# Kernel tuning notes

Measured on AMD Instinct MI355X. Metric: run time of the kernel, lower is better.

## Reference

```python
import jax, jax.numpy as jnp
import numpy as np

N_NODES = 8192
NNZ = 131072

def spmm(idx, vals, M):
    # sparse (n,n) @ dense (n,m) -> (n,m) via edge-list gather + segment-sum
    rows, cols = idx[0], idx[1]
    return jax.ops.segment_sum(vals[:, None] * M[cols], rows, num_segments=N_NODES)

def gw_conv(A_list, X, Z, W):
    # X: (B, d, n) node features; Z: (n, dz); W: (d, out)
    B, d, n = X.shape
    X0 = X.reshape(-1, n)          # (B*d, n)
    Xt = X0.T                      # (n, B*d)
    total_t = Xt                   # sum over Chebyshev-order slices (batched path sums concat dim)
    for idx, vals in A_list:
        X1t = spmm(idx, vals, Xt)                 # order-1 diffusion
        X2t = 2.0 * spmm(idx, vals, X1t) - Xt     # Chebyshev order-2 recursion
        total_t = total_t + X1t + X2t
    # adaptive dense attention adjacency, softmax over dim 0 (columns)
    Az = jax.nn.softmax(jax.nn.relu(Z @ Z.T), axis=0)  # (n, n)
    total_t = total_t + Az @ Xt
    Xr = total_t.T.reshape(B, d, n).transpose(0, 2, 1)  # (B, n, d)
    return Xr @ W                                       # (B, n, out)

def setup_inputs() -> dict:
    key = jax.random.key(0)
    ks = jax.random.split(key, 8)
    d_in, h0, h1 = 64, 128, 128
    inp = {
        "A1_indices": jax.random.randint(ks[0], (2, NNZ), 0, N_NODES, dtype=jnp.int64) if jax.config.jax_enable_x64 else jax.random.randint(ks[0], (2, NNZ), 0, N_NODES, dtype=jnp.int32),
        "A1_values": jax.random.uniform(ks[1], (NNZ,), dtype=jnp.float32),
        "A2_indices": jax.random.randint(ks[2], (2, NNZ), 0, N_NODES, dtype=jnp.int32),
        "A2_values": jax.random.uniform(ks[3], (NNZ,), dtype=jnp.float32),
        "X": jax.random.normal(ks[4], (8, d_in, N_NODES), dtype=jnp.float32),
        "Z": jax.random.normal(ks[5], (N_NODES, 64), dtype=jnp.float32),
        "W1": jax.random.normal(ks[6], (d_in, h0), dtype=jnp.float32) / np.sqrt(h0),
        "W2": jax.random.normal(ks[7], (h0, h1), dtype=jnp.float32) / np.sqrt(h1),
    }
    return inp

def reference(A1_indices, A1_values, A2_indices, A2_values, X, Z, W1, W2):
    A = [(A1_indices, A1_values), (A2_indices, A2_values)]
    H = jax.nn.relu(gw_conv(A, X, Z, W1).transpose(0, 2, 1))  # (B, h0, n)
    H = jax.nn.relu(gw_conv(A, H, Z, W2).transpose(0, 2, 1))  # (B, h1, n)
    return H.mean(axis=2)                                     # aggregate over nodes -> (B, h1)
```

## Files before the change

kernel.cpp:

```cpp
#include <hip/hip_runtime.h>


#define NN 8192
#define NNZE 131072
#define CSHIFT 48.0f

typedef float4 f4;
typedef __attribute__((ext_vector_type(8))) short bf16x8;
typedef __attribute__((ext_vector_type(4))) float f32x4;

typedef __attribute__((address_space(3))) short lds_short;
typedef __attribute__((address_space(1))) const short glb_short;

struct P8s { short* p[8]; };

__device__ inline short f2b(float x){
  unsigned u = __float_as_uint(x);
  unsigned r = (u + 0x7fffu + ((u >> 16) & 1u)) >> 16;
  return (short)r;
}
__device__ inline float b2f(unsigned short b){
  return __uint_as_float(((unsigned)b) << 16);
}

__global__ __launch_bounds__(256) void k_count2(const int* __restrict__ i1, const int* __restrict__ i2,
                                                int* __restrict__ c1, int* __restrict__ c2){
  int e = blockIdx.x*256 + threadIdx.x;
  if (blockIdx.y == 0) atomicAdd(&c1[i1[e]], 1);
  else                 atomicAdd(&c2[i2[e]], 1);
}

__global__ __launch_bounds__(1024) void k_scan2(const int* __restrict__ cnt1, const int* __restrict__ cnt2,
                                                int* __restrict__ ptr1, int* __restrict__ ptr2,
                                                int* __restrict__ cur1, int* __restrict__ cur2){
  __shared__ int sums[1024];
  const int* cnt = blockIdx.x ? cnt2 : cnt1;
  int* ptr = blockIdx.x ? ptr2 : ptr1;
  int* cur = blockIdx.x ? cur2 : cur1;
  int t = threadIdx.x;
  int loc[8]; int s = 0;
  #pragma unroll
  for (int i=0;i<8;i++){ loc[i]=s; s += cnt[t*8+i]; }
  sums[t]=s; __syncthreads();
  for (int off=1; off<1024; off<<=1){
    int v = (t>=off) ? sums[t-off] : 0;
    __syncthreads();
    sums[t] += v;
    __syncthreads();
  }
  int excl = sums[t]-s;
  #pragma unroll
  for (int i=0;i<8;i++){ int v = excl + loc[i]; ptr[t*8+i] = v; cur[t*8+i] = v; }
  if (t==1023) ptr[NN] = sums[1023];
}

__global__ __launch_bounds__(256) void k_fill2(const int* __restrict__ i1, const float* __restrict__ v1,
                                               const int* __restrict__ i2, const float* __restrict__ v2,
                                               int* __restrict__ cur1, int* __restrict__ cur2,
                                               int* __restrict__ cidx1, float* __restrict__ cval1,
                                               int* __restrict__ cidx2, float* __restrict__ cval2){
  int e = blockIdx.x*256 + threadIdx.x;
  const int* idx; const float* vals; int* cur; int* cidx; float* cval;
  if (blockIdx.y == 0){ idx=i1; vals=v1; cur=cur1; cidx=cidx1; cval=cval1; }
  else                { idx=i2; vals=v2; cur=cur2; cidx=cidx2; cval=cval2; }
  int r = idx[e], c = idx[NNZE+e];
  int p = atomicAdd(&cur[r], 1);
  cidx[p] = c; cval[p] = vals[e];
}

template<int R>
__global__ __launch_bounds__(256) void k_transb(const float* __restrict__ src, short* __restrict__ dstb){
  __shared__ float tile[32][33];
  int tx = threadIdx.x & 31, ty = threadIdx.x >> 5;
  int j0 = blockIdx.x*32, f0 = blockIdx.y*32;
  #pragma unroll
  for (int u=0;u<32;u+=8) tile[ty+u][tx] = src[(size_t)(f0+ty+u)*NN + j0+tx];
  __syncthreads();
  #pragma unroll
  for (int u=0;u<32;u+=8) dstb[(size_t)(j0+ty+u)*R + f0+tx] = f2b(tile[tx][ty+u]);
}

__global__ __launch_bounds__(256) void k_zb(const float* __restrict__ Z, short* __restrict__ Zb){
  int i = blockIdx.x*256 + threadIdx.x;
  Zb[i] = f2b(Z[i]);
}

__global__ __launch_bounds__(256) void k_wt(const float* __restrict__ W1, const float* __restrict__ W2,
                                            short* __restrict__ W1t, short* __restrict__ W2t){
  int t = threadIdx.x;
  if (blockIdx.x == 0){
    for (int i=t; i<64*128; i+=256){ int k=i>>7, o=i&127; W1t[o*64+k] = f2b(W1[i]); }
  } else {
    for (int i=t; i<128*128; i+=256){ int k=i>>7, o=i&127; W2t[o*128+k] = f2b(W2[i]); }
  }
}

__global__ __launch_bounds__(512) void k_colsum_mfma(const short* __restrict__ Zb, float* __restrict__ sb){
  int t = threadIdx.x;
  int w = t >> 6, l = t & 63;
  int lo = l & 15, g = l >> 4;
  int j = blockIdx.x*128 + w*16 + lo;
  const bf16x8* Zb8 = (const bf16x8*)Zb;
  bf16x8 bj0 = Zb8[j*8 + g];
  bf16x8 bj1 = Zb8[j*8 + g + 4];
  int i0 = blockIdx.y * (NN/8);
  float sum = 0.f;
  for (int i = i0; i < i0 + NN/8; i += 16){
    bf16x8 a0 = Zb8[(size_t)(i+lo)*8 + g];
    bf16x8 a1 = Zb8[(size_t)(i+lo)*8 + g + 4];
    f32x4 s = (f32x4){0.f,0.f,0.f,0.f};
    s = __builtin_amdgcn_mfma_f32_16x16x32_bf16(a0, bj0, s, 0,0,0);
    s = __builtin_amdgcn_mfma_f32_16x16x32_bf16(a1, bj1, s, 0,0,0);
    #pragma unroll
    for (int r=0;r<4;r++) sum += __expf(s[r] - CSHIFT);
  }
  sum += __shfl_xor(sum, 16);
  sum += __shfl_xor(sum, 32);
  if (g == 0) atomicAdd(sb + j, sum);
}

__global__ __launch_bounds__(256) void k_scaleb(const float* __restrict__ X, const float* __restrict__ sb,
                                                short* __restrict__ Yt){
  int i = blockIdx.x*256 + threadIdx.x;
  int node4 = i & (NN/4 - 1);
  f4 x = ((const f4*)X)[i];
  f4 sv = ((const f4*)sb)[node4];
  short4 o;
  o.x = f2b(x.x*(1.0f/sv.x)); o.y = f2b(x.y*(1.0f/sv.y));
  o.z = f2b(x.z*(1.0f/sv.z)); o.w = f2b(x.w*(1.0f/sv.w));
  ((short4*)Yt)[i] = o;
}

template<int F, int MODE>
__global__ __launch_bounds__(512, 4) void k_fused(
    const short* __restrict__ Zb, const short* __restrict__ YS, P8s pp, int ksize, int kzbase, int nattn,
    const int* __restrict__ ptr1, const int* __restrict__ cidx1, const float* __restrict__ cval1,
    const int* __restrict__ ptr2, const int* __restrict__ cidx2, const float* __restrict__ cval2,
    const short* __restrict__ g1, const short* __restrict__ g2, const short* __restrict__ gy,
    short* __restrict__ so1, short* __restrict__ so2, float* __restrict__ T)
{
  __shared__ __align__(16) short zk[2][32*64];
  __shared__ __align__(16) short yt[2][256*32];
  __shared__ __align__(16) short p_lds[128*40];
  int t = threadIdx.x;

  if ((int)blockIdx.x < nattn){
    constexpr int NBY = F/256;
    int id0 = blockIdx.x;
    int id = (id0 & 7)*32 + (id0 >> 3);
    int bx = id & 63, rest = id >> 6;
    int m0 = bx * 128;
    int n0 = (rest % NBY) * 256;
    int kz = kzbase + rest / NBY;
    int kbeg = kz * ksize, kend = kbeg + ksize;
    int w = t >> 6, l = t & 63;
    int lo = l & 15, g = l >> 4;
    int wm = w >> 2, wn = w & 3;

    const bf16x8* Zb8 = (const bf16x8*)Zb;
    int zirow = m0 + w*16 + lo;
    bf16x8 ziA0 = Zb8[(size_t)zirow*8 + g];
    bf16x8 ziA1 = Zb8[(size_t)zirow*8 + g + 4];

    f32x4 acc[4][4];
    #pragma unroll
    for (int i=0;i<4;i++)
      #pragma unroll
      for (int j=0;j<4;j++) acc[i][j] = (f32x4){0.f,0.f,0.f,0.f};

    auto STAGE = [&](int b, int kk){
      if (t < 256){
        int r = t >> 3, c = t & 7;
        const short* src = Zb + (((size_t)(kk + r)) << 6) + ((c ^ (r & 7)) << 3);
        __builtin_amdgcn_global_load_lds((glb_short*)src, (lds_short*)&zk[b][t*8], 16, 0, 0);
      }
      #pragma unroll
      for (int p=0;p<2;p++){
        int cc = p*512 + t;
        int r = cc >> 2, c = cc & 3;
        const short* src = YS + (size_t)(n0 + r)*NN + kk + ((c ^ ((r >> 1) & 3)) << 3);
        __builtin_amdgcn_global_load_lds((glb_short*)src, (lds_short*)&yt[b][cc*8], 16, 0, 0);
      }
    };

    STAGE(0, kbeg);

    int cur = 0;
    for (int k0 = kbeg; k0 < kend; k0 += 32){
      asm volatile("s_waitcnt vmcnt(0)" ::: "memory");
      __builtin_amdgcn_s_barrier();
      __builtin_amdgcn_sched_barrier(0);
      if (k0 + 32 < kend) STAGE(cur ^ 1, k0 + 32);
      int xa = g ^ (lo & 7), xb = (g + 4) ^ (lo & 7);
      bf16x8 b00 = *(const bf16x8*)&zk[cur][(lo*8 + xa)*8];
      bf16x8 b01 = *(const bf16x8*)&zk[cur][(lo*8 + xb)*8];
      bf16x8 b10 = *(const bf16x8*)&zk[cur][((16+lo)*8 + xa)*8];
      bf16x8 b11 = *(const bf16x8*)&zk[cur][((16+lo)*8 + xb)*8];
      f32x4 s0 = (f32x4){0.f,0.f,0.f,0.f};
      f32x4 s1 = (f32x4){0.f,0.f,0.f,0.f};
      s0 = __builtin_amdgcn_mfma_f32_16x16x32_bf16(ziA0, b00, s0, 0,0,0);
      s0 = __builtin_amdgcn_mfma_f32_16x16x32_bf16(ziA1, b01, s0, 0,0,0);
      s1 = __builtin_amdgcn_mfma_f32_16x16x32_bf16(ziA0, b10, s1, 0,0,0);
      s1 = __builtin_amdgcn_mfma_f32_16x16x32_bf16(ziA1, b11, s1, 0,0,0);
      int prow = w*16 + g*4;
      #pragma unroll
      for (int r=0;r<4;r++){
        p_lds[(prow+r)*40 + lo]      = f2b(__expf(s0[r] - CSHIFT));
        p_lds[(prow+r)*40 + 16 + lo] = f2b(__expf(s1[r] - CSHIFT));
      }
      asm volatile("s_waitcnt lgkmcnt(0)" ::: "memory");
      __builtin_amdgcn_s_barrier();
      bf16x8 aP[4];
      #pragma unroll
      for (int mf=0; mf<4; mf++)
        aP[mf] = *(const bf16x8*)&p_lds[(wm*64 + mf*16 + lo)*40 + g*8];
      __builtin_amdgcn_s_setprio(1);
      #pragma unroll
      for (int nf=0; nf<4; nf++){
        int nl = wn*64 + nf*16 + lo;
        bf16x8 bY = *(const bf16x8*)&yt[cur][(nl*4 + (g ^ ((nl >> 1) & 3)))*8];
        #pragma unroll
        for (int mf=0; mf<4; mf++)
          acc[mf][nf] = __builtin_amdgcn_mfma_f32_16x16x32_bf16(aP[mf], bY, acc[mf][nf], 0,0,0);
      }
      __builtin_amdgcn_s_setprio(0);
      cur ^= 1;
    }
    short* outp = pp.p[kz];
    #pragma unroll
    for (int mf=0; mf<4; mf++){
      int row = m0 + wm*64 + mf*16 + g*4;
      #pragma unroll
      for (int nf=0; nf<4; nf++){
        int col = n0 + wn*64 + nf*16 + lo;
        #pragma unroll
        for (int r=0;r<4;r++)
          outp[(size_t)(row+r)*F + col] = f2b(acc[mf][nf][r]);
      }
    }
  } else {
    constexpr int LPR = F/8;
    constexpr int RPB = 512/LPR;
    int gid = blockIdx.x - nattn;
    int ts = t % LPR, rl = t / LPR;
    if (MODE == 0){
      constexpr int M = NN/RPB;
      int mat = gid / M;
      int blk = gid - mat*M;
      const int*   ptr  = mat ? ptr2  : ptr1;
      const int*   cidx = mat ? cidx2 : cidx1;
      const float* cval = mat ? cval2 : cval1;
      short* outb = mat ? so2 : so1;
      int r = blk*RPB + rl;
      const bf16x8* Y8 = (const bf16x8*)g1;
      int p0 = ptr[r], p1 = ptr[r+1];
      float a[8];
      #pragma unroll
      for (int j=0;j<8;j++) a[j]=0.f;
      int p = p0;
      for (; p+7 < p1; p += 8){
        int   c[8]; float v[8]; bf16x8 x[8];
        #pragma unroll
        for (int q=0;q<8;q++){ c[q]=cidx[p+q]; v[q]=cval[p+q]; }
        #pragma unroll
        for (int q=0;q<8;q++) x[q] = Y8[(size_t)c[q]*LPR + ts];
        #pragma unroll
        for (int q=0;q<8;q++)
          #pragma unroll
          for (int j=0;j<8;j++) a[j] += v[q]*b2f((unsigned short)x[q][j]);
      }
      for (; p < p1; ++p){
        int c0 = cidx[p]; float v0 = cval[p];
        bf16x8 x0 = Y8[(size_t)c0*LPR + ts];
        #pragma unroll
        for (int j=0;j<8;j++) a[j] += v0*b2f((unsigned short)x0[j]);
      }
      bf16x8 o;
      #pragma unroll
      for (int j=0;j<8;j++) o[j] = f2b(a[j]);
      ((bf16x8*)outb)[(size_t)r*LPR + ts] = o;
    } else {
      int r = gid*RPB + rl;
      const bf16x8* Xa = (const bf16x8*)g1;
      const bf16x8* Xb = (const bf16x8*)g2;
      float a[8];
      #pragma unroll
      for (int j=0;j<8;j++) a[j]=0.f;
      {
        int p0 = ptr1[r], p1 = ptr1[r+1];
        int p = p0;
        for (; p+7 < p1; p += 8){
          int   c[8]; float v[8]; bf16x8 x[8];
          #pragma unroll
          for (int q=0;q<8;q++){ c[q]=cidx1[p+q]; v[q]=cval1[p+q]; }
          #pragma unroll
          for (int q=0;q<8;q++) x[q] = Xa[(size_t)c[q]*LPR + ts];
          #pragma unroll
          for (int q=0;q<8;q++)
            #pragma unroll
            for (int j=0;j<8;j++) a[j] += v[q]*b2f((unsigned short)x[q][j]);
        }
        for (; p < p1; ++p){
          int c0 = cidx1[p]; float v0 = cval1[p];
          bf16x8 x0 = Xa[(size_t)c0*LPR + ts];
          #pragma unroll
          for (int j=0;j<8;j++) a[j] += v0*b2f((unsigned short)x0[j]);
        }
      }
      {
        int p0 = ptr2[r], p1 = ptr2[r+1];
        int p = p0;
        for (; p+7 < p1; p += 8){
          int   c[8]; float v[8]; bf16x8 x[8];
          #pragma unroll
          for (int q=0;q<8;q++){ c[q]=cidx2[p+q]; v[q]=cval2[p+q]; }
          #pragma unroll
          for (int q=0;q<8;q++) x[q] = Xb[(size_t)c[q]*LPR + ts];
          #pragma unroll
          for (int q=0;q<8;q++)
            #pragma unroll
            for (int j=0;j<8;j++) a[j] += v[q]*b2f((unsigned short)x[q][j]);
        }
        for (; p < p1; ++p){
          int c0 = cidx2[p]; float v0 = cval2[p];
          bf16x8 x0 = Xb[(size_t)c0*LPR + ts];
          #pragma unroll
          for (int j=0;j<8;j++) a[j] += v0*b2f((unsigned short)x0[j]);
        }
      }
      bf16x8 sa = Xa[(size_t)r*LPR + ts];
      bf16x8 sbv = Xb[(size_t)r*LPR + ts];
      bf16x8 yv = ((const bf16x8*)gy)[(size_t)r*LPR + ts];
      float o[8];
      #pragma unroll
      for (int j=0;j<8;j++)
        o[j] = 2.f*a[j] + b2f((unsigned short)sa[j]) + b2f((unsigned short)sbv[j]) - b2f((unsigned short)yv[j]);
      size_t o4 = ((size_t)r*F + ts*8) >> 2;
      ((f4*)T)[o4]   = (f4){o[0],o[1],o[2],o[3]};
      ((f4*)T)[o4+1] = (f4){o[4],o[5],o[6],o[7]};
    }
  }
}

__global__ __launch_bounds__(512) void k_headm_mfma(
    const float* __restrict__ T, P8s parts, const short* __restrict__ W1t,
    const float* __restrict__ sbv, short* __restrict__ Hb, short* __restrict__ Yt)
{
  __shared__ __align__(16) short hl[128*136];
  __shared__ float rsl[128];
  int t = threadIdx.x;
  int j0 = blockIdx.x*128, b = blockIdx.y;
  for (int u = t; u < 1024; u += 512){
    int row = u >> 3, c = u & 7;
    size_t base = (size_t)(j0+row)*512 + b*64 + c*8;
    f4 x0 = *(const f4*)(T + base);
    f4 x1 = *(const f4*)(T + base + 4);
    float v[8] = {x0.x,x0.y,x0.z,x0.w,x1.x,x1.y,x1.z,x1.w};
    #pragma unroll
    for (int j=0;j<4;j++){
      bf16x8 p = *(const bf16x8*)(parts.p[j] + base);
      #pragma unroll
      for (int q=0;q<8;q++) v[q] += b2f((unsigned short)p[q]);
    }
    bf16x8 o;
    #pragma unroll
    for (int q=0;q<8;q++) o[q] = f2b(v[q]);
    *(bf16x8*)&hl[(row*8 + (c ^ (row & 7)))*8] = o;
  }
  if (t < 128) rsl[t] = 1.0f / sbv[j0 + t];
  __syncthreads();
  int w = t >> 6, l = t & 63, lo = l & 15, g = l >> 4;
  int arow = w*16 + lo;
  f32x4 acc[8];
  #pragma unroll
  for (int nf=0;nf<8;nf++) acc[nf] = (f32x4){0.f,0.f,0.f,0.f};
  #pragma unroll
  for (int ks=0; ks<2; ks++){
    bf16x8 aA = *(const bf16x8*)&hl[(arow*8 + ((ks*4+g) ^ (arow & 7)))*8];
    #pragma unroll
    for (int nf=0; nf<8; nf++){
      bf16x8 bW = *(const bf16x8*)(W1t + (size_t)(nf*16+lo)*64 + ks*32 + g*8);
      acc[nf] = __builtin_amdgcn_mfma_f32_16x16x32_bf16(aA, bW, acc[nf], 0,0,0);
    }
  }
  __syncthreads();
  int m = w*16 + g*4;
  #pragma unroll
  for (int nf=0; nf<8; nf++){
    int o = nf*16 + lo;
    #pragma unroll
    for (int r=0;r<4;r++){
      short hv = f2b(fmaxf(acc[nf][r], 0.f));
      hl[o*136 + m + r] = hv;
      Hb[(size_t)(j0+m+r)*1024 + b*128 + o] = hv;
    }
  }
  __syncthreads();
  for (int u = t; u < 2048; u += 512){
    int o = u >> 4, m8 = (u & 15)*8;
    bf16x8 hv = *(const bf16x8*)&hl[o*136 + m8];
    bf16x8 ov;
    #pragma unroll
    for (int q=0;q<8;q++) ov[q] = f2b(b2f((unsigned short)hv[q]) * rsl[m8+q]);
    *(bf16x8*)(Yt + (size_t)(b*128+o)*NN + j0 + m8) = ov;
  }
}

__global__ __launch_bounds__(512) void k_heads_mfma(
    const float* __restrict__ T, P8s parts, const short* __restrict__ W2t,
    const float* __restrict__ W2unused, float* __restrict__ out)
{
  __shared__ __align__(16) short al[128*16*8];
  __shared__ float red[8*128];
  int t = threadIdx.x;
  int j0 = blockIdx.x*128, b = blockIdx.y;
  for (int u = t; u < 2048; u += 512){
    int row = u >> 4, c = u & 15;
    size_t base = (size_t)(j0+row)*1024 + b*128 + c*8;
    f4 x0 = *(const f4*)(T + base);
    f4 x1 = *(const f4*)(T + base + 4);
    float v[8] = {x0.x,x0.y,x0.z,x0.w,x1.x,x1.y,x1.z,x1.w};
    #pragma unroll
    for (int j=0;j<2;j++){
      bf16x8 p = *(const bf16x8*)(parts.p[j] + base);
      #pragma unroll
      for (int q=0;q<8;q++) v[q] += b2f((unsigned short)p[q]);
    }
    bf16x8 o;
    #pragma unroll
    for (int q=0;q<8;q++) o[q] = f2b(v[q]);
    *(bf16x8*)&al[(row*16 + (c ^ (row & 7)))*8] = o;
  }
  __syncthreads();
  int w = t >> 6, l = t & 63, lo = l & 15, g = l >> 4;
  int arow = w*16 + lo;
  f32x4 acc[8];
  #pragma unroll
  for (int nf=0;nf<8;nf++) acc[nf] = (f32x4){0.f,0.f,0.f,0.f};
  #pragma unroll
  for (int ks=0; ks<4; ks++){
    bf16x8 aA = *(const bf16x8*)&al[(arow*16 + ((ks*4+g) ^ (arow & 7)))*8];
    #pragma unroll
    for (int nf=0; nf<8; nf++){
      bf16x8 bW = *(const bf16x8*)(W2t + (size_t)(nf*16+lo)*128 + ks*32 + g*8);
      acc[nf] = __builtin_amdgcn_mfma_f32_16x16x32_bf16(aA, bW, acc[nf], 0,0,0);
    }
  }
  #pragma unroll
  for (int nf=0; nf<8; nf++){
    float s = fmaxf(acc[nf][0],0.f) + fmaxf(acc[nf][1],0.f)
            + fmaxf(acc[nf][2],0.f) + fmaxf(acc[nf][3],0.f);
    s += __shfl_xor(s, 16);
    s += __shfl_xor(s, 32);
    if (g == 0) red[w*128 + nf*16 + lo] = s;
  }
  __syncthreads();
  if (t < 128){
    float tot = 0.f;
    #pragma unroll
    for (int ww=0; ww<8; ww++) tot += red[ww*128 + t];
    atomicAdd(&out[b*128 + t], tot * (1.0f/8192.0f));
  }
}

extern "C" void kernel_launch(void* const* d_in, const int* in_sizes, int n_in,
                              void* d_out, int out_size, void* d_ws, size_t ws_size,
                              hipStream_t stream){
  const int*   A1i = (const int*)d_in[0];
  const float* A1v = (const float*)d_in[1];
  const int*   A2i = (const int*)d_in[2];
  const float* A2v = (const float*)d_in[3];
  const float* X   = (const float*)d_in[4];
  const float* Z   = (const float*)d_in[5];
  const float* W1  = (const float*)d_in[6];
  const float* W2  = (const float*)d_in[7];
  float* out = (float*)d_out;

  char* w = (char*)d_ws;
  size_t off = 0;
  auto alloc = [&](size_t b)->char* {
    char* p = w + off;
    off += (b + 1023) & ~(size_t)1023;
    return p;
  };
  const size_t MB = 1024*1024;
  float* sb    = (float*)alloc(NN*4);
  int*   ptr1  = (int*)  alloc((NN+1)*4);
  int*   ptr2  = (int*)  alloc((NN+1)*4);
  int*   cnt   = (int*)  alloc(2*NN*4);
  int*   cur1  = (int*)  alloc(NN*4);
  int*   cur2  = (int*)  alloc(NN*4);
  int*   cidx1 = (int*)  alloc(NNZE*4);
  float* cval1 = (float*)alloc(NNZE*4);
  int*   cidx2 = (int*)  alloc(NNZE*4);
  float* cval2 = (float*)alloc(NNZE*4);
  short* Zbf   = (short*)alloc((size_t)NN*64*2);
  short* W1t   = (short*)alloc(128*64*2);
  short* W2t   = (short*)alloc(128*128*2);
  short* XT1b  = (short*)alloc((size_t)NN*512*2);
  short* BUFA  = (short*)alloc((size_t)NN*1024*2);
  short* BUFB  = (short*)alloc((size_t)NN*1024*2);
  short* HTb   = (short*)alloc((size_t)NN*1024*2);
  short* YS    = (short*)alloc((size_t)NN*1024*2);
  float* T1    = (float*)alloc((size_t)NN*512*4);
  float* T2    = (float*)alloc((size_t)NN*1024*4);
  char*  PART  = alloc((size_t)32*MB);
  (void)ws_size;
  int* cnt1 = cnt;
  int* cnt2 = cnt + NN;

  hipMemsetAsync(cnt, 0, 2*NN*4, stream);
  k_count2<<<dim3(NNZE/256, 2), 256, 0, stream>>>(A1i, A2i, cnt1, cnt2);
  k_scan2<<<2, 1024, 0, stream>>>(cnt1, cnt2, ptr1, ptr2, cur1, cur2);
  k_fill2<<<dim3(NNZE/256, 2), 256, 0, stream>>>(A1i, A1v, A2i, A2v, cur1, cur2,
                                                 cidx1, cval1, cidx2, cval2);

  k_zb<<<NN*64/256, 256, 0, stream>>>(Z, Zbf);
  k_wt<<<2, 256, 0, stream>>>(W1, W2, W1t, W2t);
  hipMemsetAsync(sb, 0, NN*4, stream);
  hipMemsetAsync(out, 0, 1024*4, stream);
  k_colsum_mfma<<<dim3(NN/128, 8), 512, 0, stream>>>(Zbf, sb);
  k_transb<512><<<dim3(NN/32, 512/32), 256, 0, stream>>>(X, XT1b);
  k_scaleb<<<512*NN/4/256, 256, 0, stream>>>(X, sb, YS);

  P8s pp1{};
  for (int i=0;i<4;i++) pp1.p[i] = (short*)(PART + (size_t)i*8*MB);
  k_fused<512,0><<<256 + 2048, 512, 0, stream>>>(Zbf, YS, pp1, NN/4, 0, 256,
      ptr1, cidx1, cval1, ptr2, cidx2, cval2,
      XT1b, nullptr, nullptr, BUFA, BUFB, nullptr);
  k_fused<512,1><<<256 + 1024, 512, 0, stream>>>(Zbf, YS, pp1, NN/4, 2, 256,
      ptr1, cidx1, cval1, ptr2, cidx2, cval2,
      BUFA, BUFB, XT1b, nullptr, nullptr, T1);
  k_headm_mfma<<<dim3(NN/128, 8), 512, 0, stream>>>(T1, pp1, W1t, sb, HTb, YS);

  P8s pp2{};
  pp2.p[0] = (short*)PART;
  pp2.p[1] = (short*)(PART + (size_t)16*MB);
  k_fused<1024,0><<<256 + 4096, 512, 0, stream>>>(Zbf, YS, pp2, NN/2, 0, 256,
      ptr1, cidx1, cval1, ptr2, cidx2, cval2,
      HTb, nullptr, nullptr, BUFA, BUFB, nullptr);
  k_fused<1024,1><<<256 + 2048, 512, 0, stream>>>(Zbf, YS, pp2, NN/2, 1, 256,
      ptr1, cidx1, cval1, ptr2, cidx2, cval2,
      BUFA, BUFB, HTb, nullptr, nullptr, T2);
  k_heads_mfma<<<dim3(NN/128, 8), 512, 0, stream>>>(T2, pp2, W2t, W2, out);
}
```

Baseline: 545.4 us.

## Merge preprocessing kernels, halve layer-1 attention K-split, use packed bf16 convert

```diff
diff --git a/kernel.cpp b/kernel.cpp
--- a/kernel.cpp
+++ b/kernel.cpp
@@ -23,11 +23,16 @@
   return __uint_as_float(((unsigned)b) << 16);
 }
 
-__global__ __launch_bounds__(256) void k_count2(const int* __restrict__ i1, const int* __restrict__ i2,
-                                                int* __restrict__ c1, int* __restrict__ c2){
+__global__ __launch_bounds__(256) void k_pre1(const int* __restrict__ i1, const int* __restrict__ i2,
+                                              int* __restrict__ c1, int* __restrict__ c2,
+                                              const float* __restrict__ Z, short* __restrict__ Zb){
   int e = blockIdx.x*256 + threadIdx.x;
-  if (blockIdx.y == 0) atomicAdd(&c1[i1[e]], 1);
-  else                 atomicAdd(&c2[i2[e]], 1);
+  if (blockIdx.y == 0)      atomicAdd(&c1[i1[e]], 1);
+  else if (blockIdx.y == 1) atomicAdd(&c2[i2[e]], 1);
+  else {
+    #pragma unroll
+    for (int q=0;q<4;q++){ int i = q*NNZE + e; Zb[i] = f2b(Z[i]); }
+  }
 }
 
 __global__ __launch_bounds__(1024) void k_scan2(const int* __restrict__ cnt1, const int* __restrict__ cnt2,
@@ -54,77 +59,71 @@
   if (t==1023) ptr[NN] = sums[1023];
 }
 
-__global__ __launch_bounds__(256) void k_fill2(const int* __restrict__ i1, const float* __restrict__ v1,
-                                               const int* __restrict__ i2, const float* __restrict__ v2,
-                                               int* __restrict__ cur1, int* __restrict__ cur2,
-                                               int* __restrict__ cidx1, float* __restrict__ cval1,
-                                               int* __restrict__ cidx2, float* __restrict__ cval2){
-  int e = blockIdx.x*256 + threadIdx.x;
-  const int* idx; const float* vals; int* cur; int* cidx; float* cval;
-  if (blockIdx.y == 0){ idx=i1; vals=v1; cur=cur1; cidx=cidx1; cval=cval1; }
-  else                { idx=i2; vals=v2; cur=cur2; cidx=cidx2; cval=cval2; }
-  int r = idx[e], c = idx[NNZE+e];
-  int p = atomicAdd(&cur[r], 1);
-  cidx[p] = c; cval[p] = vals[e];
-}
-
-template<int R>
-__global__ __launch_bounds__(256) void k_transb(const float* __restrict__ src, short* __restrict__ dstb){
+__global__ __launch_bounds__(512) void k_pre3(
+    const int* __restrict__ i1, const float* __restrict__ v1,
+    const int* __restrict__ i2, const float* __restrict__ v2,
+    int* __restrict__ cur1, int* __restrict__ cur2,
+    int* __restrict__ cidx1, float* __restrict__ cval1,
+    int* __restrict__ cidx2, float* __restrict__ cval2,
+    const short* __restrict__ Zb, float* __restrict__ sbv,
+    const float* __restrict__ X, short* __restrict__ XT1b,
+    const float* __restrict__ W1, const float* __restrict__ W2,
+    short* __restrict__ W1t, short* __restrict__ W2t)
+{
   __shared__ float tile[32][33];
-  int tx = threadIdx.x & 31, ty = threadIdx.x >> 5;
-  int j0 = blockIdx.x*32, f0 = blockIdx.y*32;
-  #pragma unroll
-  for (int u=0;u<32;u+=8) tile[ty+u][tx] = src[(size_t)(f0+ty+u)*NN + j0+tx];
-  __syncthreads();
-  #pragma unroll
-  for (int u=0;u<32;u+=8) dstb[(size_t)(j0+ty+u)*R + f0+tx] = f2b(tile[tx][ty+u]);
-}
-
-__global__ __launch_bounds__(256) void k_zb(const float* __restrict__ Z, short* __restrict__ Zb){
-  int i = blockIdx.x*256 + threadIdx.x;
-  Zb[i] = f2b(Z[i]);
-}
-
-__global__ __launch_bounds__(256) void k_wt(const float* __restrict__ W1, const float* __restrict__ W2,
-                                            short* __restrict__ W1t, short* __restrict__ W2t){
-  int t = threadIdx.x;
-  if (blockIdx.x == 0){
-    for (int i=t; i<64*128; i+=256){ int k=i>>7, o=i&127; W1t[o*64+k] = f2b(W1[i]); }
+  int bx = blockIdx.x, t = threadIdx.x;
+  if (bx < 512){
+    const int* idx; const float* vals; int* cur; int* cidx; float* cval; int e;
+    if (bx < 256){ idx=i1; vals=v1; cur=cur1; cidx=cidx1; cval=cval1; e = bx*512 + t; }
+    else         { idx=i2; vals=v2; cur=cur2; cidx=cidx2; cval=cval2; e = (bx-256)*512 + t; }
+    int r = idx[e], c = idx[NNZE+e];
+    int p = atomicAdd(&cur[r], 1);
+    cidx[p] = c; cval[p] = vals[e];
+  } else if (bx < 1024){
+    int cid = bx - 512;
+    int jblk = cid & 63, iblk = cid >> 6;
+    int w = t >> 6, l = t & 63;
+    int lo = l & 15, g = l >> 4;
+    int j = jblk*128 + w*16 + lo;
+    const bf16x8* Zb8 = (const bf16x8*)Zb;
+    bf16x8 bj0 = Zb8[j*8 + g];
+    bf16x8 bj1 = Zb8[j*8 + g + 4];
+    int i0 = iblk * (NN/8);
+    float sum = 0.f;
+    for (int i = i0; i < i0 + NN/8; i += 16){
+      bf16x8 a0 = Zb8[(size_t)(i+lo)*8 + g];
+      bf16x8 a1 = Zb8[(size_t)(i+lo)*8 + g + 4];
+      f32x4 s = (f32x4){0.f,0.f,0.f,0.f};
+      s = __builtin_amdgcn_mfma_f32_16x16x32_bf16(a0, bj0, s, 0,0,0);
+      s = __builtin_amdgcn_mfma_f32_16x16x32_bf16(a1, bj1, s, 0,0,0);
+      #pragma unroll
+      for (int r=0;r<4;r++) sum += __expf(s[r] - CSHIFT);
+    }
+    sum += __shfl_xor(sum, 16);
+    sum += __shfl_xor(sum, 32);
+    if (g == 0) atomicAdd(sbv + j, sum);
+  } else if (bx < 5120){
+    int tid = bx - 1024;
+    int j0 = (tid & 255)*32, f0 = (tid >> 8)*32;
+    int tx = t & 31, ty = t >> 5;
+    #pragma unroll
+    for (int u=0;u<32;u+=16) tile[ty+u][tx] = X[(size_t)(f0+ty+u)*NN + j0+tx];
+    __syncthreads();
+    #pragma unroll
+    for (int u=0;u<32;u+=16) XT1b[(size_t)(j0+ty+u)*512 + f0+tx] = f2b(tile[tx][ty+u]);
+  } else if (bx == 5120){
+    for (int i=t; i<64*128; i+=512){ int k=i>>7, o=i&127; W1t[o*64+k] = f2b(W1[i]); }
   } else {
-    for (int i=t; i<128*128; i+=256){ int k=i>>7, o=i&127; W2t[o*128+k] = f2b(W2[i]); }
-  }
-}
-
-__global__ __launch_bounds__(512) void k_colsum_mfma(const short* __restrict__ Zb, float* __restrict__ sb){
-  int t = threadIdx.x;
-  int w = t >> 6, l = t & 63;
-  int lo = l & 15, g = l >> 4;
-  int j = blockIdx.x*128 + w*16 + lo;
-  const bf16x8* Zb8 = (const bf16x8*)Zb;
-  bf16x8 bj0 = Zb8[j*8 + g];
-  bf16x8 bj1 = Zb8[j*8 + g + 4];
-  int i0 = blockIdx.y * (NN/8);
-  float sum = 0.f;
-  for (int i = i0; i < i0 + NN/8; i += 16){
-    bf16x8 a0 = Zb8[(size_t)(i+lo)*8 + g];
-    bf16x8 a1 = Zb8[(size_t)(i+lo)*8 + g + 4];
-    f32x4 s = (f32x4){0.f,0.f,0.f,0.f};
-    s = __builtin_amdgcn_mfma_f32_16x16x32_bf16(a0, bj0, s, 0,0,0);
-    s = __builtin_amdgcn_mfma_f32_16x16x32_bf16(a1, bj1, s, 0,0,0);
-    #pragma unroll
-    for (int r=0;r<4;r++) sum += __expf(s[r] - CSHIFT);
-  }
-  sum += __shfl_xor(sum, 16);
-  sum += __shfl_xor(sum, 32);
-  if (g == 0) atomicAdd(sb + j, sum);
-}
-
-__global__ __launch_bounds__(256) void k_scaleb(const float* __restrict__ X, const float* __restrict__ sb,
+    for (int i=t; i<128*128; i+=512){ int k=i>>7, o=i&127; W2t[o*128+k] = f2b(W2[i]); }
+  }
+}
+
+__global__ __launch_bounds__(256) void k_scaleb(const float* __restrict__ X, const float* __restrict__ sbv,
                                                 short* __restrict__ Yt){
   int i = blockIdx.x*256 + threadIdx.x;
   int node4 = i & (NN/4 - 1);
   f4 x = ((const f4*)X)[i];
-  f4 sv = ((const f4*)sb)[node4];
+  f4 sv = ((const f4*)sbv)[node4];
   short4 o;
   o.x = f2b(x.x*(1.0f/sv.x)); o.y = f2b(x.y*(1.0f/sv.y));
   o.z = f2b(x.z*(1.0f/sv.z)); o.w = f2b(x.w*(1.0f/sv.w));
@@ -147,7 +146,7 @@
   if ((int)blockIdx.x < nattn){
     constexpr int NBY = F/256;
     int id0 = blockIdx.x;
-    int id = (id0 & 7)*32 + (id0 >> 3);
+    int id = (id0 & 7)*(nattn >> 3) + (id0 >> 3);
     int bx = id & 63, rest = id >> 6;
     int m0 = bx * 128;
     int n0 = (rest % NBY) * 256;
@@ -205,8 +204,12 @@
       int prow = w*16 + g*4;
       #pragma unroll
       for (int r=0;r<4;r++){
-        p_lds[(prow+r)*40 + lo]      = f2b(__expf(s0[r] - CSHIFT));
-        p_lds[(prow+r)*40 + 16 + lo] = f2b(__expf(s1[r] - CSHIFT));
+        float e0f = __expf(s0[r] - CSHIFT);
+        float e1f = __expf(s1[r] - CSHIFT);
+        unsigned u;
+        asm("v_cvt_pk_bf16_f32 %0, %1, %2" : "=v"(u) : "v"(e0f), "v"(e1f));
+        p_lds[(prow+r)*40 + lo]      = (short)(u & 0xffffu);
+        p_lds[(prow+r)*40 + 16 + lo] = (short)(u >> 16);
       }
       asm volatile("s_waitcnt lgkmcnt(0)" ::: "memory");
       __builtin_amdgcn_s_barrier();
@@ -329,12 +332,12 @@
         }
       }
       bf16x8 sa = Xa[(size_t)r*LPR + ts];
-      bf16x8 sbv = Xb[(size_t)r*LPR + ts];
+      bf16x8 sbx = Xb[(size_t)r*LPR + ts];
       bf16x8 yv = ((const bf16x8*)gy)[(size_t)r*LPR + ts];
       float o[8];
       #pragma unroll
       for (int j=0;j<8;j++)
-        o[j] = 2.f*a[j] + b2f((unsigned short)sa[j]) + b2f((unsigned short)sbv[j]) - b2f((unsigned short)yv[j]);
+        o[j] = 2.f*a[j] + b2f((unsigned short)sa[j]) + b2f((unsigned short)sbx[j]) - b2f((unsigned short)yv[j]);
       size_t o4 = ((size_t)r*F + ts*8) >> 2;
       ((f4*)T)[o4]   = (f4){o[0],o[1],o[2],o[3]};
       ((f4*)T)[o4+1] = (f4){o[4],o[5],o[6],o[7]};
@@ -357,7 +360,7 @@
     f4 x1 = *(const f4*)(T + base + 4);
     float v[8] = {x0.x,x0.y,x0.z,x0.w,x1.x,x1.y,x1.z,x1.w};
     #pragma unroll
-    for (int j=0;j<4;j++){
+    for (int j=0;j<2;j++){
       bf16x8 p = *(const bf16x8*)(parts.p[j] + base);
       #pragma unroll
       for (int q=0;q<8;q++) v[q] += b2f((unsigned short)p[q]);
@@ -408,7 +411,7 @@
 
 __global__ __launch_bounds__(512) void k_heads_mfma(
     const float* __restrict__ T, P8s parts, const short* __restrict__ W2t,
-    const float* __restrict__ W2unused, float* __restrict__ out)
+    float* __restrict__ out)
 {
   __shared__ __align__(16) short al[128*16*8];
   __shared__ float red[8*128];
@@ -510,25 +513,22 @@
   int* cnt2 = cnt + NN;
 
   hipMemsetAsync(cnt, 0, 2*NN*4, stream);
-  k_count2<<<dim3(NNZE/256, 2), 256, 0, stream>>>(A1i, A2i, cnt1, cnt2);
-  k_scan2<<<2, 1024, 0, stream>>>(cnt1, cnt2, ptr1, ptr2, cur1, cur2);
-  k_fill2<<<dim3(NNZE/256, 2), 256, 0, stream>>>(A1i, A1v, A2i, A2v, cur1, cur2,
-                                                 cidx1, cval1, cidx2, cval2);
-
-  k_zb<<<NN*64/256, 256, 0, stream>>>(Z, Zbf);
-  k_wt<<<2, 256, 0, stream>>>(W1, W2, W1t, W2t);
   hipMemsetAsync(sb, 0, NN*4, stream);
   hipMemsetAsync(out, 0, 1024*4, stream);
-  k_colsum_mfma<<<dim3(NN/128, 8), 512, 0, stream>>>(Zbf, sb);
-  k_transb<512><<<dim3(NN/32, 512/32), 256, 0, stream>>>(X, XT1b);
+  k_pre1<<<dim3(NNZE/256, 3), 256, 0, stream>>>(A1i, A2i, cnt1, cnt2, Z, Zbf);
+  k_scan2<<<2, 1024, 0, stream>>>(cnt1, cnt2, ptr1, ptr2, cur1, cur2);
+  k_pre3<<<5122, 512, 0, stream>>>(A1i, A1v, A2i, A2v, cur1, cur2,
+                                   cidx1, cval1, cidx2, cval2,
+                                   Zbf, sb, X, XT1b, W1, W2, W1t, W2t);
   k_scaleb<<<512*NN/4/256, 256, 0, stream>>>(X, sb, YS);
 
   P8s pp1{};
-  for (int i=0;i<4;i++) pp1.p[i] = (short*)(PART + (size_t)i*8*MB);
-  k_fused<512,0><<<256 + 2048, 512, 0, stream>>>(Zbf, YS, pp1, NN/4, 0, 256,
+  pp1.p[0] = (short*)PART;
+  pp1.p[1] = (short*)(PART + (size_t)8*MB);
+  k_fused<512,0><<<128 + 2048, 512, 0, stream>>>(Zbf, YS, pp1, NN/2, 0, 128,
       ptr1, cidx1, cval1, ptr2, cidx2, cval2,
       XT1b, nullptr, nullptr, BUFA, BUFB, nullptr);
-  k_fused<512,1><<<256 + 1024, 512, 0, stream>>>(Zbf, YS, pp1, NN/4, 2, 256,
+  k_fused<512,1><<<128 + 1024, 512, 0, stream>>>(Zbf, YS, pp1, NN/2, 1, 128,
       ptr1, cidx1, cval1, ptr2, cidx2, cval2,
       BUFA, BUFB, XT1b, nullptr, nullptr, T1);
   k_headm_mfma<<<dim3(NN/128, 8), 512, 0, stream>>>(T1, pp1, W1t, sb, HTb, YS);
@@ -542,5 +542,5 @@
   k_fused<1024,1><<<256 + 2048, 512, 0, stream>>>(Zbf, YS, pp2, NN/2, 1, 256,
       ptr1, cidx1, cval1, ptr2, cidx2, cval2,
       BUFA, BUFB, HTb, nullptr, nullptr, T2);
-  k_heads_mfma<<<dim3(NN/128, 8), 512, 0, stream>>>(T2, pp2, W2t, W2, out);
-}
+  k_heads_mfma<<<dim3(NN/128, 8), 512, 0, stream>>>(T2, pp2, W2t, out);
+}
```

Result: slower. 626.0 us (+14.8%).
